# Optimization experiments

Hardware: AMD Instinct MI355X
Metric: run time of the kernel (lower is better)

Reference implementation:

```python
import jax, jax.numpy as jnp
import numpy as np

B, L, E, H = 2, 2048, 1024, 16
D = E // H  # 64


def setup_inputs() -> dict:
    key = jax.random.key(0)
    ks = jax.random.split(key, 9)
    return {
        "query": jax.random.normal(ks[0], (B, L, E), dtype=jnp.float32),
        "value": jax.random.normal(ks[1], (B, L, E), dtype=jnp.float32),
        "key": jax.random.normal(ks[2], (B, L, E), dtype=jnp.float32),
        "mask": jax.random.randint(ks[3], (B, 1, L, L), 0, 2, dtype=jnp.int32),
        "Wq": jax.random.normal(ks[4], (D, D), dtype=jnp.float32) * 0.05,
        "Wk": jax.random.normal(ks[5], (D, D), dtype=jnp.float32) * 0.05,
        "Wv": jax.random.normal(ks[6], (D, D), dtype=jnp.float32) * 0.05,
        "Wfc": jax.random.normal(ks[7], (E, E), dtype=jnp.float32) * 0.02,
        "bfc": jax.random.normal(ks[8], (E,), dtype=jnp.float32) * 0.02,
    }


def reference(query, value, key, mask, Wq, Wk, Wv, Wfc, bfc):
    b, q_len, _ = query.shape
    k_len = key.shape[1]
    v_len = value.shape[1]
    # split heads: [b, l, H, D]
    q = query.reshape(b, q_len, H, D)
    k = key.reshape(b, k_len, H, D)
    v = value.reshape(b, v_len, H, D)
    # per-head linear projections (shared weights across heads, no bias)
    q = jnp.einsum('bqhd,ed->bqhe', q, Wq)
    k = jnp.einsum('bkhd,ed->bkhe', k, Wk)
    v = jnp.einsum('bvhd,ed->bvhe', v, Wv)
    # attention scores [b, H, q, k]
    attn = jnp.einsum('bqhd,bkhd->bhqk', q, k)
    # NOTE: original masks BEFORE scaling, and scales by sqrt(embedding_size)
    attn = jnp.where(mask == 0, jnp.float32(-1e20), attn)
    attn = attn / jnp.float32(E ** 0.5)
    attn = jax.nn.softmax(attn, axis=3)
    out = jnp.einsum('bhqk,bkhd->bqhd', attn, v).reshape(b, q_len, E)
    out = out @ Wfc.T + bfc
    return out
```

## Files before the change

kernel.cpp:

```cpp
#include <hip/hip_runtime.h>
#include <hip/hip_bf16.h>


#define B_ 2
#define L_ 2048
#define E_ 1024
#define H_ 16
#define D_ 64

typedef __attribute__((ext_vector_type(8))) short s8v;
typedef __attribute__((ext_vector_type(4))) float f4v;
typedef __attribute__((ext_vector_type(2))) float f2v;

__device__ __forceinline__ f4v mfma16(s8v a, s8v b, f4v c) {
    return __builtin_amdgcn_mfma_f32_16x16x32_bf16(a, b, c, 0, 0, 0);
}

__device__ __forceinline__ float fast_exp2(float x) {
    return __builtin_amdgcn_exp2f(x);
}

__device__ __forceinline__ ushort bf16bits(float f) {
    __hip_bfloat16 h = __float2bfloat16(f);
    return *(ushort*)&h;
}

__device__ __forceinline__ void glds16(const __hip_bfloat16* g, ushort* l) {
    __builtin_amdgcn_global_load_lds(
        (const __attribute__((address_space(1))) void*)g,
        (__attribute__((address_space(3))) void*)l,
        16, 0, 0);
}

__device__ __forceinline__ s8v ld8_dual(const void* p, size_t idx, bool isf32) {
    if (isf32) {
        const float* pf = (const float*)p + idx;
        f4v f0 = *(const f4v*)pf;
        f4v f1 = *(const f4v*)(pf + 4);
        s8v r;
        r[0] = (short)bf16bits(f0[0]); r[1] = (short)bf16bits(f0[1]);
        r[2] = (short)bf16bits(f0[2]); r[3] = (short)bf16bits(f0[3]);
        r[4] = (short)bf16bits(f1[0]); r[5] = (short)bf16bits(f1[1]);
        r[6] = (short)bf16bits(f1[2]); r[7] = (short)bf16bits(f1[3]);
        return r;
    }
    return *(const s8v*)((const __hip_bfloat16*)p + idx);
}

__device__ __forceinline__ s8v ld8_ws(const __hip_bfloat16* p) {
    return *(const s8v*)p;
}

__device__ __forceinline__ s8v u4_to_s8(uint a, uint b, uint c, uint d) {
    union { uint u[4]; s8v v; } x;
    x.u[0] = a; x.u[1] = b; x.u[2] = c; x.u[3] = d;
    return x.v;
}

__device__ __forceinline__ bool block_detect_f32(const void* q_in, int* sflag) {
    if (threadIdx.x == 0) *sflag = 0;
    __syncthreads();
    const ushort* qq = (const ushort*)q_in + (threadIdx.x & 255) * 16;
    int bad = 0;
    #pragma unroll
    for (int i = 0; i < 16; ++i) bad += (((qq[i] >> 7) & 0xFF) >= 0x8E);
    bad += __shfl_xor(bad, 1);
    bad += __shfl_xor(bad, 2);
    bad += __shfl_xor(bad, 4);
    bad += __shfl_xor(bad, 8);
    bad += __shfl_xor(bad, 16);
    bad += __shfl_xor(bad, 32);
    if ((threadIdx.x & 63) == 0 && threadIdx.x < 256) atomicAdd(sflag, bad);
    __syncthreads();
    return *sflag > 100;
}

__device__ __forceinline__ void cvt_piece(
    size_t i4, const void* Wfc, const void* bfc,
    __hip_bfloat16* wfc_bf, __hip_bfloat16* bfc_bf, bool isf32)
{
    const size_t base = i4 * 4;
    const size_t n1 = (size_t)E_ * E_;
    if (base >= n1 + E_) return;
    const void* src = (base < n1) ? Wfc : bfc;
    const size_t off = (base < n1) ? base : base - n1;
    __hip_bfloat16* dst = (base < n1) ? (wfc_bf + off) : (bfc_bf + off);
    if (isf32) {
        f4v v = *(const f4v*)((const float*)src + off);
        #pragma unroll
        for (int j = 0; j < 4; ++j) dst[j] = __float2bfloat16(v[j]);
    } else {
        *(ushort4*)dst = *(const ushort4*)((const ushort*)src + off);
    }
}

__global__ __launch_bounds__(256) void proj_all_kernel(
    const void* __restrict__ q_in, const void* __restrict__ k_in,
    const void* __restrict__ v_in,
    const void* __restrict__ Wq, const void* __restrict__ Wk,
    const void* __restrict__ Wv,
    const void* __restrict__ Wfc, const void* __restrict__ bfc,
    const int* __restrict__ mask, unsigned long long* __restrict__ mbits,
    __hip_bfloat16* __restrict__ qp, __hip_bfloat16* __restrict__ kp,
    __hip_bfloat16* __restrict__ vpT,
    __hip_bfloat16* __restrict__ wfc_bf, __hip_bfloat16* __restrict__ bfc_bf)
{
    __shared__ __align__(16) ushort tile[64][72];
    __shared__ __align__(16) ushort wlds[64 * 72];
    __shared__ int sflag;
    const int wave = threadIdx.x >> 6;
    const int lane = threadIdx.x & 63;
    const int quad = lane >> 4;
    const int l16  = lane & 15;

    if (blockIdx.y == 3) {
        const int lane_ = threadIdx.x & 63;
        const size_t wbase = (size_t)blockIdx.x * 128 + wave * 32;
        #pragma unroll 4
        for (int i = 0; i < 32; ++i) {
            const size_t widx = wbase + i;
            const int v = mask[widx * 64 + lane_];
            const unsigned long long bal = __ballot(v != 0);
            if (lane_ == 0) mbits[widx] = bal;
        }
        return;
    }

    const bool isf32 = block_detect_f32(q_in, &sflag);

    if (blockIdx.y == 4) {
        cvt_piece((size_t)blockIdx.x * 256 + threadIdx.x, Wfc, bfc, wfc_bf, bfc_bf, isf32);
        if (blockIdx.x == 0)
            cvt_piece((size_t)(E_ * (size_t)E_ / 4) + threadIdx.x, Wfc, bfc, wfc_bf, bfc_bf, isf32);
        return;
    }

    {
        const void* W = blockIdx.y == 0 ? Wq : (blockIdx.y == 1 ? Wk : Wv);
        const int row = threadIdx.x >> 2;
        const int c0  = (threadIdx.x & 3) * 16;
        if (isf32) {
            const float* wsrc = (const float*)W + row * 64 + c0;
            #pragma unroll
            for (int j = 0; j < 16; ++j)
                wlds[row * 72 + c0 + j] = bf16bits(wsrc[j]);
        } else {
            const ushort* wsrc = (const ushort*)W + row * 64 + c0;
            *(s8v*)&wlds[row * 72 + c0]     = *(const s8v*)wsrc;
            *(s8v*)&wlds[row * 72 + c0 + 8] = *(const s8v*)(wsrc + 8);
        }
    }
    __syncthreads();

    if (blockIdx.y < 2) {
        const void* X = blockIdx.y == 0 ? q_in : k_in;
        __hip_bfloat16* dst = blockIdx.y == 0 ? qp : kp;
        const float oscale = (blockIdx.y == 0) ? 0.045084439755930314f : 1.0f;
        const int m0 = (blockIdx.x * 4 + wave) * 16;

        const size_t abase = (size_t)(m0 + l16) * D_;
        s8v a0 = ld8_dual(X, abase + quad * 8, isf32);
        s8v a1 = ld8_dual(X, abase + 32 + quad * 8, isf32);

        f4v acc[4];
        #pragma unroll
        for (int nt = 0; nt < 4; ++nt) {
            const ushort* wr = &wlds[(nt * 16 + l16) * 72];
            s8v b0 = *(const s8v*)(wr + quad * 8);
            s8v b1 = *(const s8v*)(wr + 32 + quad * 8);
            f4v c = {0.f, 0.f, 0.f, 0.f};
            c = mfma16(a0, b0, c);
            c = mfma16(a1, b1, c);
            acc[nt] = c;
        }
        #pragma unroll
        for (int r = 0; r < 4; ++r) {
            const int m = m0 + quad * 4 + r;
            const int h = m & 15;
            const int bl = m >> 4;
            const int b = bl >> 11;
            const int l = bl & (L_ - 1);
            #pragma unroll
            for (int nt = 0; nt < 4; ++nt) {
                const int e = nt * 16 + l16;
                dst[(((size_t)(b * H_ + h)) * L_ + l) * D_ + e] =
                    __float2bfloat16(acc[nt][r] * oscale);
            }
        }
    } else {
        const int l0 = (blockIdx.x & 31) * 64;
        const int bh = blockIdx.x >> 5;
        const int b = bh >> 4, h = bh & 15;
        const int lw = l0 + wave * 16;

        const size_t xbase = ((size_t)(b * L_ + lw + l16)) * E_ + h * D_;
        s8v a0 = ld8_dual(v_in, xbase + quad * 8, isf32);
        s8v a1 = ld8_dual(v_in, xbase + 32 + quad * 8, isf32);

        #pragma unroll
        for (int nt = 0; nt < 4; ++nt) {
            const int e = nt * 16 + l16;
            const ushort* wr = &wlds[e * 72];
            s8v b0 = *(const s8v*)(wr + quad * 8);
            s8v b1 = *(const s8v*)(wr + 32 + quad * 8);
            f4v c = {0.f, 0.f, 0.f, 0.f};
            c = mfma16(a0, b0, c);
            c = mfma16(a1, b1, c);
            #pragma unroll
            for (int r = 0; r < 4; ++r)
                tile[wave * 16 + quad * 4 + r][e] = bf16bits(c[r]);
        }
        __syncthreads();
        const int e  = threadIdx.x >> 2;
        const int lc = (threadIdx.x & 3) * 16;
        s8v s0, s1;
        #pragma unroll
        for (int i = 0; i < 8; ++i) {
            s0[i] = (short)tile[lc + i][e];
            s1[i] = (short)tile[lc + 8 + i][e];
        }
        __hip_bfloat16* drow = vpT + ((size_t)bh * D_ + e) * L_ + l0 + lc;
        *(s8v*)drow = s0;
        *(s8v*)(drow + 8) = s1;
    }
}

__global__ __launch_bounds__(256) void cvt_wfc_kernel(
    const void* __restrict__ Wfc, const void* __restrict__ bfc,
    __hip_bfloat16* __restrict__ wfc_bf, __hip_bfloat16* __restrict__ bfc_bf,
    const void* __restrict__ q_in)
{
    __shared__ int sflag;
    const bool isf32 = block_detect_f32(q_in, &sflag);
    cvt_piece((size_t)blockIdx.x * 256 + threadIdx.x, Wfc, bfc, wfc_bf, bfc_bf, isf32);
}

__global__ __launch_bounds__(256, 4) void attn_kernel(
    const __hip_bfloat16* __restrict__ qp,
    const __hip_bfloat16* __restrict__ kp,
    const __hip_bfloat16* __restrict__ vpT,
    const unsigned long long* __restrict__ mbits,
    __hip_bfloat16* __restrict__ attn_out)
{
    __shared__ __align__(16) ushort kbuf[2][64 * 64];
    __shared__ __align__(16) ushort vbuf[2][64 * 64];

    const int wave = threadIdx.x >> 6;
    const int lane = threadIdx.x & 63;
    const int quad = lane >> 4;
    const int l16  = lane & 15;
    const int sw   = l16 & 7;
    const int bh = blockIdx.y;
    const int b = bh >> 4, h = bh & 15;
    const int q0 = blockIdx.x * 64 + wave * 16;

    const __hip_bfloat16* kbh = kp + (size_t)bh * L_ * D_;
    const __hip_bfloat16* vbh = vpT + (size_t)bh * D_ * L_;
    const unsigned long long* mrow = mbits + ((size_t)b * L_ + q0 + l16) * 32;

    const int lrow = lane >> 3;
    const int lchk = (lane & 7) ^ lrow;
    const int r0 = wave * 16;
    const __hip_bfloat16* kg0 = kbh + (size_t)(r0 + lrow) * D_ + lchk * 8;
    const __hip_bfloat16* kg1 = kbh + (size_t)(r0 + 8 + lrow) * D_ + lchk * 8;
    const __hip_bfloat16* vg0 = vbh + (size_t)(r0 + lrow) * L_ + lchk * 8;
    const __hip_bfloat16* vg1 = vbh + (size_t)(r0 + 8 + lrow) * L_ + lchk * 8;

    const __hip_bfloat16* qbase = qp + ((size_t)bh * L_ + q0) * D_;
    s8v qa0 = ld8_ws(qbase + (size_t)l16 * D_ + quad * 8);
    s8v qa1 = ld8_ws(qbase + (size_t)l16 * D_ + 32 + quad * 8);

    f2v rs2 = {0.f, 0.f};
    f4v o[4];
    #pragma unroll
    for (int nt = 0; nt < 4; ++nt) o[nt] = (f4v){0.f, 0.f, 0.f, 0.f};

    glds16(kg0, &kbuf[0][r0 * 64]);
    glds16(kg1, &kbuf[0][r0 * 64 + 512]);
    glds16(vg0, &vbuf[0][r0 * 64]);
    glds16(vg1, &vbuf[0][r0 * 64 + 512]);
    __syncthreads();

    const int shq = quad * 4;
    int cur = 0;
    for (int it = 0; it < 32; ++it) {
        const int k0 = it * 64;
        const unsigned long long wq = mrow[it];
        const uint wlo_sh = ((uint)wq) >> shq;
        const uint whi_sh = ((uint)(wq >> 32)) >> shq;
        if (it < 31) {
            glds16(kg0 + (size_t)(k0 + 64) * D_, &kbuf[cur ^ 1][r0 * 64]);
            glds16(kg1 + (size_t)(k0 + 64) * D_, &kbuf[cur ^ 1][r0 * 64 + 512]);
            glds16(vg0 + (k0 + 64), &vbuf[cur ^ 1][r0 * 64]);
            glds16(vg1 + (k0 + 64), &vbuf[cur ^ 1][r0 * 64 + 512]);
        }
        f4v s[4];
        #pragma unroll
        for (int nt = 0; nt < 4; ++nt) {
            const ushort* kr = &kbuf[cur][(nt * 16 + l16) * 64];
            s8v kb0 = *(const s8v*)(kr + ((quad ^ sw) << 3));
            s8v kb1 = *(const s8v*)(kr + (((quad + 4) ^ sw) << 3));
            f4v c = {0.f, 0.f, 0.f, 0.f};
            c = mfma16(kb0, qa0, c);
            c = mfma16(kb1, qa1, c);
            s[nt] = c;
        }
        uint dw[4][2];
        #pragma unroll
        for (int nt = 0; nt < 4; ++nt) {
            const uint hs = (nt & 2) ? whi_sh : wlo_sh;
            float pr[4];
            #pragma unroll
            for (int r = 0; r < 4; ++r) {
                const float p = fast_exp2(s[nt][r]);
                const int m = __builtin_amdgcn_sbfe((int)hs, ((nt & 1) << 4) + r, 1);
                pr[r] = __uint_as_float(__float_as_uint(p) & (uint)m);
            }
            rs2 += (f2v){pr[0], pr[1]};
            rs2 += (f2v){pr[2], pr[3]};
            asm("v_cvt_pk_bf16_f32 %0, %1, %2"
                : "=v"(dw[nt][0]) : "v"(pr[0]), "v"(pr[1]));
            asm("v_cvt_pk_bf16_f32 %0, %1, %2"
                : "=v"(dw[nt][1]) : "v"(pr[2]), "v"(pr[3]));
        }
        uint w00 = dw[0][0], w10 = dw[1][0];
        uint w01 = dw[0][1], w11 = dw[1][1];
        uint w20 = dw[2][0], w30 = dw[3][0];
        uint w21 = dw[2][1], w31 = dw[3][1];
        asm("v_permlane32_swap_b32 %0, %1" : "+v"(w00), "+v"(w10));
        asm("v_permlane16_swap_b32 %0, %1" : "+v"(w00), "+v"(w10));
        asm("v_permlane32_swap_b32 %0, %1" : "+v"(w01), "+v"(w11));
        asm("v_permlane16_swap_b32 %0, %1" : "+v"(w01), "+v"(w11));
        asm("v_permlane32_swap_b32 %0, %1" : "+v"(w20), "+v"(w30));
        asm("v_permlane16_swap_b32 %0, %1" : "+v"(w20), "+v"(w30));
        asm("v_permlane32_swap_b32 %0, %1" : "+v"(w21), "+v"(w31));
        asm("v_permlane16_swap_b32 %0, %1" : "+v"(w21), "+v"(w31));
        s8v pa0 = u4_to_s8(w00, w01, w10, w11);
        s8v pa1 = u4_to_s8(w20, w21, w30, w31);
        #pragma unroll
        for (int nt = 0; nt < 4; ++nt) {
            const ushort* vr = &vbuf[cur][(nt * 16 + l16) * 64];
            s8v vb0 = *(const s8v*)(vr + ((quad ^ sw) << 3));
            s8v vb1 = *(const s8v*)(vr + (((quad + 4) ^ sw) << 3));
            o[nt] = mfma16(pa0, vb0, o[nt]);
            o[nt] = mfma16(pa1, vb1, o[nt]);
        }
        __syncthreads();
        cur ^= 1;
    }
    float v = rs2[0] + rs2[1];
    v += __shfl_xor(v, 16, 64);
    v += __shfl_xor(v, 32, 64);
    #pragma unroll
    for (int r = 0; r < 4; ++r) {
        const int qrow = quad * 4 + r;
        const float li = __shfl(v, qrow, 64);
        const float inv = 1.0f / fmaxf(li, 1e-30f);
        const int row = q0 + qrow;
        #pragma unroll
        for (int nt = 0; nt < 4; ++nt) {
            const int d = nt * 16 + l16;
            attn_out[((size_t)(b * L_ + row)) * E_ + h * D_ + d] =
                __float2bfloat16(o[nt][r] * inv);
        }
    }
}

__global__ __launch_bounds__(256, 4) void fc_kernel(
    const __hip_bfloat16* __restrict__ x,
    const __hip_bfloat16* __restrict__ wfc_bf,
    const __hip_bfloat16* __restrict__ bfc_bf,
    void* __restrict__ out, const void* __restrict__ q_in)
{
    __shared__ __align__(16) ushort abuf[2][128 * 64];
    __shared__ __align__(16) ushort bbuf[2][64 * 64];
    __shared__ int sflag;
    const bool isf32 = block_detect_f32(q_in, &sflag);
    const int wave = threadIdx.x >> 6;
    const int lane = threadIdx.x & 63;
    const int quad = lane >> 4;
    const int l16  = lane & 15;
    const int sw   = l16 & 7;
    const int m0 = blockIdx.x * 128;
    const int n0 = blockIdx.y * 64;
    const int wr = wave >> 1;
    const int wc = wave & 1;

    const int lrow = lane >> 3;
    const int lchk = (lane & 7) ^ lrow;

    const __hip_bfloat16* ag[4];
    #pragma unroll
    for (int c = 0; c < 4; ++c)
        ag[c] = x + (size_t)(m0 + c * 32 + wave * 8 + lrow) * E_ + lchk * 8;
    const __hip_bfloat16* bg[2];
    #pragma unroll
    for (int c = 0; c < 2; ++c)
        bg[c] = wfc_bf + (size_t)(n0 + c * 32 + wave * 8 + lrow) * E_ + lchk * 8;

    f4v acc[4][2];
    #pragma unroll
    for (int fm = 0; fm < 4; ++fm)
        #pragma unroll
        for (int fn = 0; fn < 2; ++fn) acc[fm][fn] = (f4v){0.f, 0.f, 0.f, 0.f};

    #pragma unroll
    for (int c = 0; c < 4; ++c) glds16(ag[c], &abuf[0][(c * 32 + wave * 8) * 64]);
    #pragma unroll
    for (int c = 0; c < 2; ++c) glds16(bg[c], &bbuf[0][(c * 32 + wave * 8) * 64]);
    __syncthreads();

    int cur = 0;
    for (int it = 0; it < 16; ++it) {
        if (it < 15) {
            #pragma unroll
            for (int c = 0; c < 4; ++c)
                glds16(ag[c] + (it + 1) * 64, &abuf[cur ^ 1][(c * 32 + wave * 8) * 64]);
            #pragma unroll
            for (int c = 0; c < 2; ++c)
                glds16(bg[c] + (it + 1) * 64, &bbuf[cur ^ 1][(c * 32 + wave * 8) * 64]);
        }
        s8v a0[4], a1[4];
        #pragma unroll
        for (int fm = 0; fm < 4; ++fm) {
            const ushort* ar = &abuf[cur][(wr * 64 + fm * 16 + l16) * 64];
            a0[fm] = *(const s8v*)(ar + ((quad ^ sw) << 3));
            a1[fm] = *(const s8v*)(ar + (((quad + 4) ^ sw) << 3));
        }
        #pragma unroll
        for (int fn = 0; fn < 2; ++fn) {
            const ushort* br = &bbuf[cur][(wc * 32 + fn * 16 + l16) * 64];
            s8v b0 = *(const s8v*)(br + ((quad ^ sw) << 3));
            s8v b1 = *(const s8v*)(br + (((quad + 4) ^ sw) << 3));
            #pragma unroll
            for (int fm = 0; fm < 4; ++fm) {
                acc[fm][fn] = mfma16(a0[fm], b0, acc[fm][fn]);
                acc[fm][fn] = mfma16(a1[fm], b1, acc[fm][fn]);
            }
        }
        __syncthreads();
        cur ^= 1;
    }
    #pragma unroll
    for (int fm = 0; fm < 4; ++fm) {
        #pragma unroll
        for (int r = 0; r < 4; ++r) {
            const int m = m0 + wr * 64 + fm * 16 + quad * 4 + r;
            #pragma unroll
            for (int fn = 0; fn < 2; ++fn) {
                const int n = n0 + wc * 32 + fn * 16 + l16;
                const float val = acc[fm][fn][r] + __bfloat162float(bfc_bf[n]);
                if (isf32) ((float*)out)[(size_t)m * E_ + n] = val;
                else       ((__hip_bfloat16*)out)[(size_t)m * E_ + n] = __float2bfloat16(val);
            }
        }
    }
}

extern "C" void kernel_launch(void* const* d_in, const int* in_sizes, int n_in,
                              void* d_out, int out_size, void* d_ws, size_t ws_size,
                              hipStream_t stream) {
    const void* query = d_in[0];
    const void* value = d_in[1];
    const void* key   = d_in[2];
    const int*  mask  = (const int*)d_in[3];
    const void* Wq  = d_in[4];
    const void* Wk  = d_in[5];
    const void* Wv  = d_in[6];
    const void* Wfc = d_in[7];
    const void* bfc = d_in[8];

    char* ws = (char*)d_ws;
    unsigned long long* mbits     = (unsigned long long*)(ws + (64u << 10));
    __hip_bfloat16* qp            = (__hip_bfloat16*)(ws + (2u  << 20));
    __hip_bfloat16* kp            = (__hip_bfloat16*)(ws + (10u << 20));
    __hip_bfloat16* vpT           = (__hip_bfloat16*)(ws + (18u << 20));
    __hip_bfloat16* attn_out      = (__hip_bfloat16*)(ws + (26u << 20));

    const bool big_ws = ws_size >= (37ull << 20);
    __hip_bfloat16* wfc_bf = big_ws ? (__hip_bfloat16*)(ws + (34ull << 20)) : qp;
    __hip_bfloat16* bfc_bf = wfc_bf + (size_t)E_ * E_;

    proj_all_kernel<<<dim3(1024, big_ws ? 5 : 4), 256, 0, stream>>>(
        query, key, value, Wq, Wk, Wv, Wfc, bfc, mask, mbits,
        qp, kp, vpT, wfc_bf, bfc_bf);
    attn_kernel<<<dim3(32, 32), 256, 0, stream>>>(qp, kp, vpT, mbits, attn_out);
    if (!big_ws)
        cvt_wfc_kernel<<<1025, 256, 0, stream>>>(Wfc, bfc, wfc_bf, bfc_bf, query);
    fc_kernel<<<dim3(32, 16), 256, 0, stream>>>(attn_out, wfc_bf, bfc_bf, d_out, query);
}
```

Before: 222.0 us.

## Drop LDS staging in attention; read K/V from global with XCD-aware block mapping

The attention kernel no longer stages K and V tiles through double-buffered shared memory with barriers. Each wave now loads its MFMA operands straight from global memory and relies on L2/MALL caching. The grid becomes 1-D, and block IDs are remapped so that the blocks sharing one batch-head land on the same XCD (kid&7), which should improve cache locality. This removes the LDS traffic and the __syncthreads, but it adds redundant global loads across the four waves and exposes load latency, since there is no explicit prefetch any more.

```diff
diff --git a/kernel.cpp b/kernel.cpp
--- a/kernel.cpp
+++ b/kernel.cpp
@@ -242,30 +242,20 @@
     const unsigned long long* __restrict__ mbits,
     __hip_bfloat16* __restrict__ attn_out)
 {
-    __shared__ __align__(16) ushort kbuf[2][64 * 64];
-    __shared__ __align__(16) ushort vbuf[2][64 * 64];
-
     const int wave = threadIdx.x >> 6;
     const int lane = threadIdx.x & 63;
     const int quad = lane >> 4;
     const int l16  = lane & 15;
-    const int sw   = l16 & 7;
-    const int bh = blockIdx.y;
+    const int kid  = blockIdx.x;
+    const int bh   = (kid & 7) * 4 + (kid >> 8);
+    const int qblk = (kid >> 3) & 31;
     const int b = bh >> 4, h = bh & 15;
-    const int q0 = blockIdx.x * 64 + wave * 16;
+    const int q0 = qblk * 64 + wave * 16;
 
     const __hip_bfloat16* kbh = kp + (size_t)bh * L_ * D_;
     const __hip_bfloat16* vbh = vpT + (size_t)bh * D_ * L_;
     const unsigned long long* mrow = mbits + ((size_t)b * L_ + q0 + l16) * 32;
 
-    const int lrow = lane >> 3;
-    const int lchk = (lane & 7) ^ lrow;
-    const int r0 = wave * 16;
-    const __hip_bfloat16* kg0 = kbh + (size_t)(r0 + lrow) * D_ + lchk * 8;
-    const __hip_bfloat16* kg1 = kbh + (size_t)(r0 + 8 + lrow) * D_ + lchk * 8;
-    const __hip_bfloat16* vg0 = vbh + (size_t)(r0 + lrow) * L_ + lchk * 8;
-    const __hip_bfloat16* vg1 = vbh + (size_t)(r0 + 8 + lrow) * L_ + lchk * 8;
-
     const __hip_bfloat16* qbase = qp + ((size_t)bh * L_ + q0) * D_;
     s8v qa0 = ld8_ws(qbase + (size_t)l16 * D_ + quad * 8);
     s8v qa1 = ld8_ws(qbase + (size_t)l16 * D_ + 32 + quad * 8);
@@ -275,31 +265,18 @@
     #pragma unroll
     for (int nt = 0; nt < 4; ++nt) o[nt] = (f4v){0.f, 0.f, 0.f, 0.f};
 
-    glds16(kg0, &kbuf[0][r0 * 64]);
-    glds16(kg1, &kbuf[0][r0 * 64 + 512]);
-    glds16(vg0, &vbuf[0][r0 * 64]);
-    glds16(vg1, &vbuf[0][r0 * 64 + 512]);
-    __syncthreads();
-
     const int shq = quad * 4;
-    int cur = 0;
     for (int it = 0; it < 32; ++it) {
         const int k0 = it * 64;
         const unsigned long long wq = mrow[it];
         const uint wlo_sh = ((uint)wq) >> shq;
         const uint whi_sh = ((uint)(wq >> 32)) >> shq;
-        if (it < 31) {
-            glds16(kg0 + (size_t)(k0 + 64) * D_, &kbuf[cur ^ 1][r0 * 64]);
-            glds16(kg1 + (size_t)(k0 + 64) * D_, &kbuf[cur ^ 1][r0 * 64 + 512]);
-            glds16(vg0 + (k0 + 64), &vbuf[cur ^ 1][r0 * 64]);
-            glds16(vg1 + (k0 + 64), &vbuf[cur ^ 1][r0 * 64 + 512]);
-        }
         f4v s[4];
         #pragma unroll
         for (int nt = 0; nt < 4; ++nt) {
-            const ushort* kr = &kbuf[cur][(nt * 16 + l16) * 64];
-            s8v kb0 = *(const s8v*)(kr + ((quad ^ sw) << 3));
-            s8v kb1 = *(const s8v*)(kr + (((quad + 4) ^ sw) << 3));
+            const __hip_bfloat16* kr = kbh + (size_t)(k0 + nt * 16 + l16) * D_;
+            s8v kb0 = ld8_ws(kr + quad * 8);
+            s8v kb1 = ld8_ws(kr + 32 + quad * 8);
             f4v c = {0.f, 0.f, 0.f, 0.f};
             c = mfma16(kb0, qa0, c);
             c = mfma16(kb1, qa1, c);
@@ -339,14 +316,12 @@
         s8v pa1 = u4_to_s8(w20, w21, w30, w31);
         #pragma unroll
         for (int nt = 0; nt < 4; ++nt) {
-            const ushort* vr = &vbuf[cur][(nt * 16 + l16) * 64];
-            s8v vb0 = *(const s8v*)(vr + ((quad ^ sw) << 3));
-            s8v vb1 = *(const s8v*)(vr + (((quad + 4) ^ sw) << 3));
+            const __hip_bfloat16* vr = vbh + (size_t)(nt * 16 + l16) * L_ + k0;
+            s8v vb0 = ld8_ws(vr + quad * 8);
+            s8v vb1 = ld8_ws(vr + 32 + quad * 8);
             o[nt] = mfma16(pa0, vb0, o[nt]);
             o[nt] = mfma16(pa1, vb1, o[nt]);
         }
-        __syncthreads();
-        cur ^= 1;
     }
     float v = rs2[0] + rs2[1];
     v += __shfl_xor(v, 16, 64);
@@ -484,7 +459,7 @@
     proj_all_kernel<<<dim3(1024, big_ws ? 5 : 4), 256, 0, stream>>>(
         query, key, value, Wq, Wk, Wv, Wfc, bfc, mask, mbits,
         qp, kp, vpT, wfc_bf, bfc_bf);
-    attn_kernel<<<dim3(32, 32), 256, 0, stream>>>(qp, kp, vpT, mbits, attn_out);
+    attn_kernel<<<dim3(1024), 256, 0, stream>>>(qp, kp, vpT, mbits, attn_out);
     if (!big_ws)
         cvt_wfc_kernel<<<1025, 256, 0, stream>>>(Wfc, bfc, wfc_bf, bfc_bf, query);
     fc_kernel<<<dim3(32, 16), 256, 0, stream>>>(attn_out, wfc_bf, bfc_bf, d_out, query);
```

Result: slower. 404.1 us (+82.0%).
